# Optimization experiments

Hardware: AMD Instinct MI355X
Metric: run time of the kernel (lower is better)

The kernel has to match this reference:

```python
import jax, jax.numpy as jnp
import numpy as np

N_NODES = 20000
N_EDGES = 320000
N_GRAPHS = 256
F_IN = 128
HID = 512


def _xavier(key, shape, gain=1.0):
    fan_out, fan_in = shape
    a = gain * np.sqrt(6.0 / (fan_in + fan_out))
    return jax.random.uniform(key, shape, jnp.float32, -a, a)


def setup_inputs() -> dict:
    key = jax.random.key(0)
    ks = jax.random.split(key, 9)
    x = jax.random.normal(ks[0], (N_NODES, F_IN), jnp.float32)
    edge_index = jax.random.randint(ks[1], (2, N_EDGES), 0, N_NODES, dtype=jnp.int64)
    batch = jnp.sort(jax.random.randint(ks[2], (N_NODES,), 0, N_GRAPHS, dtype=jnp.int64))
    return {
        "x": x,
        "edge_index": edge_index,
        "batch": batch,
        "lin_W": _xavier(ks[3], (HID, F_IN)),
        "lin_b": jnp.zeros((HID,), jnp.float32),
        "W1": _xavier(ks[4], (HID, F_IN)),
        "b1": jnp.zeros((HID,), jnp.float32),
        "W2": _xavier(ks[5], (HID, HID)),
        "b2": jnp.zeros((HID,), jnp.float32),
        "W3": _xavier(ks[6], (HID, HID)),
        "b3": jnp.zeros((HID,), jnp.float32),
        "W4": _xavier(ks[7], (HID, HID)),
        "b4": jnp.zeros((HID,), jnp.float32),
    }


def _gcn_conv(x, W, b, src, dst, norm, n_nodes):
    # PyG GCNConv: h = x @ W.T; out_i = sum_j norm_ij * h_j (scatter over dst) + b
    h = x @ W.T
    msg = h[src] * norm[:, None]  # [E', H] gather + scale
    return jax.ops.segment_sum(msg, dst, num_segments=n_nodes) + b


def reference(x, edge_index, batch, lin_W, lin_b, W1, b1, W2, b2, W3, b3, W4, b4):
    n = x.shape[0]
    loop = jnp.arange(n, dtype=edge_index.dtype)
    src = jnp.concatenate([edge_index[0], loop])
    dst = jnp.concatenate([edge_index[1], loop])
    # symmetric normalization D^-1/2 (A+I) D^-1/2, degree = in-degree over dst
    deg = jax.ops.segment_sum(jnp.ones_like(src, dtype=x.dtype), dst, num_segments=n)
    dis = jnp.where(deg > 0, jax.lax.rsqrt(deg), 0.0)
    norm = dis[src] * dis[dst]

    x_l = x @ lin_W.T + lin_b  # dead code when act=None (kept for faithfulness)

    h1 = _gcn_conv(x, W1, b1, src, dst, norm, n)
    h2 = _gcn_conv(h1, W2, b2, src, dst, norm, n)
    h3 = _gcn_conv(h2, W3, b3, src, dst, norm, n)
    h4 = _gcn_conv(h3, W4, b4, src, dst, norm, n)
    h = jnp.concatenate([h1, h2, h3, h4], axis=1)  # [N, 4*HID]

    h_pooled = jax.ops.segment_max(h, batch, num_segments=N_GRAPHS)
    h_pos = (h > 0).astype(h.dtype)
    counts = jax.ops.segment_sum(jnp.ones((n,), h.dtype), batch, num_segments=N_GRAPHS)
    h_pos_pooled = jax.ops.segment_sum(h_pos, batch, num_segments=N_GRAPHS) / jnp.maximum(counts, 1.0)[:, None]
    return jnp.concatenate([h_pooled, h_pos_pooled], axis=1)  # [G, 8*HID]
```

## Files before the change

kernel.cpp:

```cpp
#include <hip/hip_runtime.h>
#include <cfloat>
#include <cmath>

#define F_IN 128
#define HID 512

typedef short bf16x8 __attribute__((ext_vector_type(8)));
typedef float f32x4 __attribute__((ext_vector_type(4)));

__device__ static inline void split_bf16(float v, short& hi, short& lo) {
    unsigned u = __float_as_uint(v);
    unsigned r = u + 0x7FFF + ((u >> 16) & 1);
    hi = (short)(r >> 16);
    float hf = __uint_as_float(((unsigned)(unsigned short)hi) << 16);
    float res = v - hf;
    unsigned u2 = __float_as_uint(res);
    unsigned r2 = u2 + 0x7FFF + ((u2 >> 16) & 1);
    lo = (short)(r2 >> 16);
}

__device__ static inline void gload_lds16(const void* g, void* l) {
    __builtin_amdgcn_global_load_lds(
        (const __attribute__((address_space(1))) unsigned int*)g,
        (__attribute__((address_space(3))) unsigned int*)l,
        16, 0, 0);
}


__global__ void zero_kernel(int* __restrict__ a, int n) {
    int i = blockIdx.x * blockDim.x + threadIdx.x;
    if (i < n) a[i] = 0;
}

__global__ void count_in_kernel(const int* __restrict__ dst, int* __restrict__ cnt, int E) {
    int e = blockIdx.x * blockDim.x + threadIdx.x;
    if (e < E) atomicAdd(&cnt[dst[e]], 1);
}

__global__ void scan_kernel(const int* __restrict__ cnt, int* __restrict__ offs, int n) {
    __shared__ int buf[1024];
    __shared__ int carry_s;
    if (threadIdx.x == 0) carry_s = 0;
    __syncthreads();
    for (int base = 0; base < n; base += 1024) {
        int i = base + threadIdx.x;
        int v = (i < n) ? cnt[i] : 0;
        buf[threadIdx.x] = v;
        __syncthreads();
        for (int s = 1; s < 1024; s <<= 1) {
            int t = (threadIdx.x >= s) ? buf[threadIdx.x - s] : 0;
            __syncthreads();
            buf[threadIdx.x] += t;
            __syncthreads();
        }
        int total = buf[1023];
        if (i < n) offs[i] = carry_s + buf[threadIdx.x] - v;
        __syncthreads();
        if (threadIdx.x == 0) carry_s += total;
        __syncthreads();
    }
    if (threadIdx.x == 0) offs[n] = carry_s;
}

__global__ void dis_starts_kernel(const int* __restrict__ offs, float* __restrict__ dis,
                                  const int* __restrict__ batch, int* __restrict__ starts,
                                  int n, int G) {
    int i = blockIdx.x * blockDim.x + threadIdx.x;
    if (i >= n) return;
    dis[i] = rsqrtf((float)(offs[i + 1] - offs[i] + 1));
    int b = batch[i];
    if (i == 0) {
        for (int g = 0; g <= b; g++) starts[g] = 0;
    } else {
        int bp = batch[i - 1];
        for (int g = bp + 1; g <= b; g++) starts[g] = i;
    }
    if (i == n - 1) {
        for (int g = b + 1; g <= G; g++) starts[g] = n;
    }
}

__global__ void fill_csr_kernel(const int* __restrict__ src, const int* __restrict__ dst,
                                const int* __restrict__ offs, int* __restrict__ cnt,
                                unsigned short* __restrict__ csr, int E) {
    int e = blockIdx.x * blockDim.x + threadIdx.x;
    if (e < E) {
        int d = dst[e];
        int p = atomicSub(&cnt[d], 1);
        csr[offs[d] + p - 1] = (unsigned short)src[e];
    }
}

__global__ void wconv_kernel(const float* __restrict__ W1, const float* __restrict__ W2,
                             const float* __restrict__ W3, const float* __restrict__ W4,
                             short* __restrict__ Whi, short* __restrict__ Wlo) {
    int i = blockIdx.x * blockDim.x + threadIdx.x;
    const int n1 = HID * F_IN, nk = HID * HID;
    float v;
    if (i < n1) v = W1[i];
    else if (i < n1 + nk) v = W2[i - n1];
    else if (i < n1 + 2 * nk) v = W3[i - n1 - nk];
    else if (i < n1 + 3 * nk) v = W4[i - n1 - 2 * nk];
    else return;
    short h, l;
    split_bf16(v, h, l);
    Whi[i] = h;
    Wlo[i] = l;
}

template <int F, int CHUNKS>
__global__ __launch_bounds__(64) void agg_chunk_kernel(
    const float* __restrict__ H, const float* __restrict__ dis,
    const int* __restrict__ offs, const unsigned short* __restrict__ csr,
    short* __restrict__ Ahi, short* __restrict__ Alo, int n) {
    int blk = blockIdx.x;
    int i = blk / CHUNKS;
    int chunk = blk % CHUNKS;
    int col = chunk * 64 + threadIdx.x;
    const float* Hc = H + col;

    float di = dis[i];
    float a = di * Hc[(size_t)i * F];
    int e = offs[i], e1 = offs[i + 1];
    for (; e + 8 <= e1; e += 8) {
        int j0 = csr[e],     j1 = csr[e + 1], j2 = csr[e + 2], j3 = csr[e + 3];
        int j4 = csr[e + 4], j5 = csr[e + 5], j6 = csr[e + 6], j7 = csr[e + 7];
        float d0 = dis[j0], d1 = dis[j1], d2 = dis[j2], d3 = dis[j3];
        float d4 = dis[j4], d5 = dis[j5], d6 = dis[j6], d7 = dis[j7];
        float r0 = Hc[(size_t)j0 * F], r1 = Hc[(size_t)j1 * F];
        float r2 = Hc[(size_t)j2 * F], r3 = Hc[(size_t)j3 * F];
        float r4 = Hc[(size_t)j4 * F], r5 = Hc[(size_t)j5 * F];
        float r6 = Hc[(size_t)j6 * F], r7 = Hc[(size_t)j7 * F];
        a += d0 * r0 + d1 * r1 + d2 * r2 + d3 * r3;
        a += d4 * r4 + d5 * r5 + d6 * r6 + d7 * r7;
    }
    for (; e < e1; e++) {
        int j = csr[e];
        a += dis[j] * Hc[(size_t)j * F];
    }
    a *= di;
    short h, l;
    split_bf16(a, h, l);
    Ahi[(size_t)i * F + col] = h;
    Alo[(size_t)i * F + col] = l;
}

__global__ __launch_bounds__(256) void gemm_mfma_kernel(
    const short* __restrict__ Ahi, const short* __restrict__ Alo,
    const short* __restrict__ Whi, const short* __restrict__ Wlo,
    const float* __restrict__ bias, float* __restrict__ C,
    int M, int K, int Nout, int MT, int MT8) {
    __shared__ __attribute__((aligned(16))) short lds[4][4096];

    int blk = blockIdx.x;
    int xcd = blk & 7;
    int r = blk >> 3;
    int n0t = r & 3;
    int mt = xcd * MT8 + (r >> 2);
    if (mt >= MT) return;
    int m0 = mt * 128, n0 = n0t * 128;

    int tid = threadIdx.x;
    int w = tid >> 6, l = tid & 63;
    int lrow = l & 15, lq = l >> 4;

    const short* gp = (w == 0) ? Ahi : (w == 1) ? Alo : (w == 2) ? Whi : Wlo;
    int base_mn = (w < 2) ? m0 : n0;

    f32x4 acc[4][4];
    #pragma unroll
    for (int i = 0; i < 4; i++)
        #pragma unroll
        for (int j = 0; j < 4; j++) acc[i][j] = (f32x4){0.f, 0.f, 0.f, 0.f};

    int wm = w >> 1, wn = w & 1;

    for (int k0 = 0; k0 < K; k0 += 32) {
        const short* gbase = gp + (size_t)(base_mn + lrow) * K + (k0 + lq * 8);
        #pragma unroll
        for (int s = 0; s < 8; s++) {
            gload_lds16(gbase + (size_t)s * 16 * K, &lds[w][s * 64 * 8]);
        }
        __syncthreads();

        bf16x8 ah[4], al[4], wh[4], wl[4];
        #pragma unroll
        for (int i = 0; i < 4; i++) {
            int sA = wm * 4 + i;
            ah[i] = *(const bf16x8*)&lds[0][(sA * 64 + l) * 8];
            al[i] = *(const bf16x8*)&lds[1][(sA * 64 + l) * 8];
            int sW = wn * 4 + i;
            wh[i] = *(const bf16x8*)&lds[2][(sW * 64 + l) * 8];
            wl[i] = *(const bf16x8*)&lds[3][(sW * 64 + l) * 8];
        }
        #pragma unroll
        for (int i = 0; i < 4; i++)
            #pragma unroll
            for (int j = 0; j < 4; j++) {
                acc[i][j] = __builtin_amdgcn_mfma_f32_16x16x32_bf16(ah[i], wh[j], acc[i][j], 0, 0, 0);
                acc[i][j] = __builtin_amdgcn_mfma_f32_16x16x32_bf16(ah[i], wl[j], acc[i][j], 0, 0, 0);
                acc[i][j] = __builtin_amdgcn_mfma_f32_16x16x32_bf16(al[i], wh[j], acc[i][j], 0, 0, 0);
            }
        __syncthreads();
    }

    #pragma unroll
    for (int j = 0; j < 4; j++) {
        int col = n0 + (wn * 4 + j) * 16 + lrow;
        float bv = bias[col];
        #pragma unroll
        for (int i = 0; i < 4; i++) {
            int mrow = m0 + (wm * 4 + i) * 16 + lq * 4;
            #pragma unroll
            for (int rr = 0; rr < 4; rr++) {
                int mm = mrow + rr;
                if (mm < M) C[(size_t)mm * Nout + col] = acc[i][j][rr] + bv;
            }
        }
    }
}

__global__ __launch_bounds__(64) void pool_kernel(
    const float* __restrict__ H, const int* __restrict__ starts,
    float* __restrict__ out, int layer) {
    int g = blockIdx.x;
    int c = blockIdx.y * 64 + threadIdx.x;
    int s = starts[g], e = starts[g + 1];
    float mx = -INFINITY;
    int pos = 0;
    #pragma unroll 4
    for (int n = s; n < e; n++) {
        float v = H[(size_t)n * HID + c];
        mx = fmaxf(mx, v);
        pos += (v > 0.0f) ? 1 : 0;
    }
    float cntf = fmaxf((float)(e - s), 1.0f);
    out[(size_t)g * (8 * HID) + layer * HID + c] = mx;
    out[(size_t)g * (8 * HID) + 4 * HID + layer * HID + c] = (float)pos / cntf;
}

extern "C" void kernel_launch(void* const* d_in, const int* in_sizes, int n_in,
                              void* d_out, int out_size, void* d_ws, size_t ws_size,
                              hipStream_t stream) {
    const float* x     = (const float*)d_in[0];
    const int*   eidx  = (const int*)d_in[1];
    const int*   batch = (const int*)d_in[2];
    const float* W1 = (const float*)d_in[5];
    const float* b1 = (const float*)d_in[6];
    const float* W2 = (const float*)d_in[7];
    const float* b2 = (const float*)d_in[8];
    const float* W3 = (const float*)d_in[9];
    const float* b3 = (const float*)d_in[10];
    const float* W4 = (const float*)d_in[11];
    const float* b4 = (const float*)d_in[12];
    float* out = (float*)d_out;

    const int N = in_sizes[0] / F_IN;
    const int E = in_sizes[1] / 2;
    const int G = out_size / (8 * HID);

    const int* src = eidx;
    const int* dst = eidx + E;

    const size_t nW = (size_t)HID * F_IN + 3 * (size_t)HID * HID;
    char* w = (char*)d_ws;
    short* Ahi = (short*)w; w += (size_t)N * HID * sizeof(short);
    short* Alo = (short*)w; w += (size_t)N * HID * sizeof(short);
    float* H   = (float*)w; w += (size_t)N * HID * sizeof(float);
    short* Whi = (short*)w; w += nW * sizeof(short);
    short* Wlo = (short*)w; w += nW * sizeof(short);
    int* offs  = (int*)w;   w += (size_t)(N + 4) * sizeof(int);
    unsigned short* csr = (unsigned short*)w; w += (size_t)E * sizeof(unsigned short);
    int* cnt   = (int*)w;   w += (size_t)N * sizeof(int);
    float* dis = (float*)w; w += (size_t)N * sizeof(float);
    int* starts = (int*)w;  w += (size_t)(G + 1) * sizeof(int);

    const size_t wo1 = 0;
    const size_t wo2 = (size_t)HID * F_IN;
    const size_t wo3 = wo2 + (size_t)HID * HID;
    const size_t wo4 = wo3 + (size_t)HID * HID;

    const int TB = 256;
    zero_kernel<<<(N + TB - 1) / TB, TB, 0, stream>>>(cnt, N);
    count_in_kernel<<<(E + TB - 1) / TB, TB, 0, stream>>>(dst, cnt, E);
    scan_kernel<<<1, 1024, 0, stream>>>(cnt, offs, N);
    dis_starts_kernel<<<(N + TB - 1) / TB, TB, 0, stream>>>(offs, dis, batch, starts, N, G);
    fill_csr_kernel<<<(E + TB - 1) / TB, TB, 0, stream>>>(src, dst, offs, cnt, csr, E);
    wconv_kernel<<<((int)nW + TB - 1) / TB, TB, 0, stream>>>(W1, W2, W3, W4, Whi, Wlo);

    const int MT = (N + 127) / 128;
    const int MT8 = (MT + 7) / 8;
    const int gemm_blocks = 8 * MT8 * 4;
    dim3 pool_grid(G, HID / 64);

    agg_chunk_kernel<F_IN, 2><<<N * 2, 64, 0, stream>>>(x, dis, offs, csr, Ahi, Alo, N);
    gemm_mfma_kernel<<<gemm_blocks, 256, 0, stream>>>(Ahi, Alo, Whi + wo1, Wlo + wo1, b1, H,
                                                      N, F_IN, HID, MT, MT8);
    pool_kernel<<<pool_grid, 64, 0, stream>>>(H, starts, out, 0);

    const size_t wos[3] = {wo2, wo3, wo4};
    const float* bs_[3] = {b2, b3, b4};
    for (int ll = 0; ll < 3; ll++) {
        agg_chunk_kernel<HID, 8><<<N * 8, 64, 0, stream>>>(H, dis, offs, csr, Ahi, Alo, N);
        gemm_mfma_kernel<<<gemm_blocks, 256, 0, stream>>>(Ahi, Alo, Whi + wos[ll], Wlo + wos[ll], bs_[ll], H,
                                                          N, HID, HID, MT, MT8);
        pool_kernel<<<pool_grid, 64, 0, stream>>>(H, starts, out, ll + 1);
    }
}
```

Baseline: 677.3 us.

## Split aggregation wavefront into two half-waves over edges with phased block ordering

The aggregation kernel now assigns each 64-lane wave a 32-column chunk. The two 32-lane halves take alternating edges, and their partial sums are combined with a cross-half shuffle. The block index is reordered so that consecutive blocks cover a group of chunks before moving to the next node, in phases across all nodes. This doubles the block count and halves the per-lane serial gather chain, aiming to add memory-level parallelism for the irregular gathers. In exchange, each half-wave reads only 128 bytes of a row per edge instead of 256, half the lanes sit idle at the store, and node rows are revisited in separate phases, which may reduce cache locality.

```diff
diff --git a/kernel.cpp b/kernel.cpp
--- a/kernel.cpp
+++ b/kernel.cpp
@@ -109,40 +109,50 @@
 }
 
 template <int F, int CHUNKS>
-__global__ __launch_bounds__(64) void agg_chunk_kernel(
+__global__ __launch_bounds__(64) void agg_phase_kernel(
     const float* __restrict__ H, const float* __restrict__ dis,
     const int* __restrict__ offs, const unsigned short* __restrict__ csr,
     short* __restrict__ Ahi, short* __restrict__ Alo, int n) {
+    constexpr int LOWB = (CHUNKS >= 8) ? 8 : CHUNKS;
+    constexpr int LB = (CHUNKS >= 8) ? 3 : 2;
     int blk = blockIdx.x;
-    int i = blk / CHUNKS;
-    int chunk = blk % CHUNKS;
-    int col = chunk * 64 + threadIdx.x;
+    int c_lo = blk & (LOWB - 1);
+    int rest = blk >> LB;
+    int p = rest / n;
+    int i = rest - p * n;
+    int chunk = p * LOWB + c_lo;
+
+    int tid = threadIdx.x;
+    int half = tid >> 5;
+    int lc = tid & 31;
+    int col = chunk * 32 + lc;
     const float* Hc = H + col;
 
     float di = dis[i];
-    float a = di * Hc[(size_t)i * F];
+    float a = (half == 0) ? di * Hc[(size_t)i * F] : 0.0f;
     int e = offs[i], e1 = offs[i + 1];
     for (; e + 8 <= e1; e += 8) {
-        int j0 = csr[e],     j1 = csr[e + 1], j2 = csr[e + 2], j3 = csr[e + 3];
-        int j4 = csr[e + 4], j5 = csr[e + 5], j6 = csr[e + 6], j7 = csr[e + 7];
+        int j0 = csr[e + half];
+        int j1 = csr[e + 2 + half];
+        int j2 = csr[e + 4 + half];
+        int j3 = csr[e + 6 + half];
         float d0 = dis[j0], d1 = dis[j1], d2 = dis[j2], d3 = dis[j3];
-        float d4 = dis[j4], d5 = dis[j5], d6 = dis[j6], d7 = dis[j7];
         float r0 = Hc[(size_t)j0 * F], r1 = Hc[(size_t)j1 * F];
         float r2 = Hc[(size_t)j2 * F], r3 = Hc[(size_t)j3 * F];
-        float r4 = Hc[(size_t)j4 * F], r5 = Hc[(size_t)j5 * F];
-        float r6 = Hc[(size_t)j6 * F], r7 = Hc[(size_t)j7 * F];
         a += d0 * r0 + d1 * r1 + d2 * r2 + d3 * r3;
-        a += d4 * r4 + d5 * r5 + d6 * r6 + d7 * r7;
-    }
-    for (; e < e1; e++) {
-        int j = csr[e];
+    }
+    for (; e + half < e1; e += 2) {
+        int j = csr[e + half];
         a += dis[j] * Hc[(size_t)j * F];
     }
+    a += __shfl_xor(a, 32, 64);
     a *= di;
-    short h, l;
-    split_bf16(a, h, l);
-    Ahi[(size_t)i * F + col] = h;
-    Alo[(size_t)i * F + col] = l;
+    if (half == 0) {
+        short h, l;
+        split_bf16(a, h, l);
+        Ahi[(size_t)i * F + col] = h;
+        Alo[(size_t)i * F + col] = l;
+    }
 }
 
 __global__ __launch_bounds__(256) void gemm_mfma_kernel(
@@ -293,7 +303,7 @@
     const int gemm_blocks = 8 * MT8 * 4;
     dim3 pool_grid(G, HID / 64);
 
-    agg_chunk_kernel<F_IN, 2><<<N * 2, 64, 0, stream>>>(x, dis, offs, csr, Ahi, Alo, N);
+    agg_phase_kernel<F_IN, 4><<<N * 4, 64, 0, stream>>>(x, dis, offs, csr, Ahi, Alo, N);
     gemm_mfma_kernel<<<gemm_blocks, 256, 0, stream>>>(Ahi, Alo, Whi + wo1, Wlo + wo1, b1, H,
                                                       N, F_IN, HID, MT, MT8);
     pool_kernel<<<pool_grid, 64, 0, stream>>>(H, starts, out, 0);
@@ -301,7 +311,7 @@
     const size_t wos[3] = {wo2, wo3, wo4};
     const float* bs_[3] = {b2, b3, b4};
     for (int ll = 0; ll < 3; ll++) {
-        agg_chunk_kernel<HID, 8><<<N * 8, 64, 0, stream>>>(H, dis, offs, csr, Ahi, Alo, N);
+        agg_phase_kernel<HID, 16><<<N * 16, 64, 0, stream>>>(H, dis, offs, csr, Ahi, Alo, N);
         gemm_mfma_kernel<<<gemm_blocks, 256, 0, stream>>>(Ahi, Alo, Whi + wos[ll], Wlo + wos[ll], bs_[ll], H,
                                                           N, HID, HID, MT, MT8);
         pool_kernel<<<pool_grid, 64, 0, stream>>>(H, starts, out, ll + 1);
```

Result: slower. 763.1 us (+12.7%).
